# Optimization experiments

Measured on AMD Instinct MI355X. Metric: run time of the kernel, lower is better.

Reference implementation:

```python
import jax, jax.numpy as jnp
import numpy as np
from jax import lax

RADIUS = 5


def setup_inputs() -> dict:
    key = jax.random.key(0)
    k1, k2 = jax.random.split(key)
    B, K, H, W = 4, 6, 128, 128
    win = 2 * RADIUS + 1
    labels = jax.random.uniform(k1, (B, K, H, W), dtype=jnp.float32)
    weights = jax.random.uniform(k2, (B, H * W, win, win), dtype=jnp.float32)
    return {"labels": labels, "weights": weights}


def reference(labels, weights):
    # labels:  [B, K, H, W]  class probabilities
    B, K, H, W = labels.shape
    win = 2 * RADIUS + 1
    N = H * W

    # Extract 11x11 patches around every pixel for all classes at once.
    patches = lax.conv_general_dilated_patches(
        labels, (win, win), (1, 1), padding=[(RADIUS, RADIUS), (RADIUS, RADIUS)]
    )
    patches = patches.reshape(B, K, win * win, N)

    w = weights.reshape(B, N, win * win)

    # sum over window of weights * P, per class: wp[b,k,n] = sum_o w[b,n,o] * patches[b,k,o,n]
    wp = jnp.einsum('bkon,bno->bkn', patches, w)

    p = labels.reshape(B, K, N)
    num = jnp.einsum('bkn,bkn->bk', p, wp)          # association
    den = jnp.einsum('bkn,bn->bk', p, w.sum(-1))    # degree
    L = num / den                                    # [B, K]

    # nn.L1Loss()(L, zeros) per class = mean_b |L[b,k]|
    losses = jnp.mean(jnp.abs(L), axis=0)            # [K]
    return K - jnp.sum(losses)
```

## Files before the change

kernel.cpp:

```cpp
#include <hip/hip_runtime.h>

#define RADIUS 5
#define WIN    11
#define WIN2   121
#define KCLS   6
#define HH     128
#define WW     128
#define BB     4
#define NPIX   (HH*WW)
#define TPB    256
#define NBLK   (BB*HH)
#define LABW   138
#define NSITE  (WIN*LABW)
#define PLSTR  (NSITE*2)

__global__ __launch_bounds__(TPB, 2) void ncut_main(
    const float* __restrict__ labels,
    const float* __restrict__ weights,
    float* __restrict__ part) {
  __shared__ float shl[3 * PLSTR];
  __shared__ float shred[4 * 12];

  const int tid = threadIdx.x;
  const int blk = blockIdx.x;
  const int b   = blk >> 7;
  const int y0  = blk & (HH - 1);

  const float* labB = labels + (size_t)b * KCLS * NPIX;
  for (int s = tid; s < NSITE; s += TPB) {
    const int tr = s / LABW;
    const int tc = s - tr * LABW;
    const int gy = y0 - RADIUS + tr;
    const int gx = tc - RADIUS;
    const bool ok = ((unsigned)gy < (unsigned)HH) & ((unsigned)gx < (unsigned)WW);
    const float* lp = labB + (size_t)gy * WW + gx;
#pragma unroll
    for (int p = 0; p < 3; ++p) {
      float2 v = make_float2(0.f, 0.f);
      if (ok) {
        v.x = lp[(size_t)(2 * p) * NPIX];
        v.y = lp[(size_t)(2 * p + 1) * NPIX];
      }
      *reinterpret_cast<float2*>(shl + p * PLSTR + 2 * s) = v;
    }
  }
  __syncthreads();

  const int px = tid >> 1;
  const int q  = tid & 1;
  const float* wr = weights +
      ((size_t)b * NPIX + (size_t)y0 * WW + px) * WIN2 + q * 60;

  float2 a0 = make_float2(0.f, 0.f);
  float2 a1 = make_float2(0.f, 0.f);
  float2 a2 = make_float2(0.f, 0.f);
  float wsum = 0.f;

#pragma unroll
  for (int g = 0; g < 15; ++g) {
    float4 wv;
    __builtin_memcpy(&wv, wr + 4 * g, 16);
#pragma unroll
    for (int m = 0; m < 4; ++m) {
      const int c  = 4 * g + m;
      const int liA = (c / WIN) * LABW + (c % WIN);
      const int liB = ((60 + c) / WIN) * LABW + ((60 + c) % WIN);
      const int li  = px + (q ? liB : liA);
      const float w = (m == 0) ? wv.x : (m == 1) ? wv.y : (m == 2) ? wv.z : wv.w;
      wsum += w;
      const float2 v0 = *reinterpret_cast<const float2*>(shl + 0 * PLSTR + 2 * li);
      const float2 v1 = *reinterpret_cast<const float2*>(shl + 1 * PLSTR + 2 * li);
      const float2 v2 = *reinterpret_cast<const float2*>(shl + 2 * PLSTR + 2 * li);
      a0.x += w * v0.x; a0.y += w * v0.y;
      a1.x += w * v1.x; a1.y += w * v1.y;
      a2.x += w * v2.x; a2.y += w * v2.y;
    }
  }
  if (q == 0) {
    const float w = wr[120];
    const int li = px + 10 * LABW + 10;
    wsum += w;
    const float2 v0 = *reinterpret_cast<const float2*>(shl + 0 * PLSTR + 2 * li);
    const float2 v1 = *reinterpret_cast<const float2*>(shl + 1 * PLSTR + 2 * li);
    const float2 v2 = *reinterpret_cast<const float2*>(shl + 2 * PLSTR + 2 * li);
    a0.x += w * v0.x; a0.y += w * v0.y;
    a1.x += w * v1.x; a1.y += w * v1.y;
    a2.x += w * v2.x; a2.y += w * v2.y;
  }

  wsum += __shfl_xor(wsum, 1);
  a0.x += __shfl_xor(a0.x, 1); a0.y += __shfl_xor(a0.y, 1);
  a1.x += __shfl_xor(a1.x, 1); a1.y += __shfl_xor(a1.y, 1);
  a2.x += __shfl_xor(a2.x, 1); a2.y += __shfl_xor(a2.y, 1);

  const int lc = px + 5 * LABW + 5;
  const float2 c0 = *reinterpret_cast<const float2*>(shl + 0 * PLSTR + 2 * lc);
  const float2 c1 = *reinterpret_cast<const float2*>(shl + 1 * PLSTR + 2 * lc);
  const float2 c2 = *reinterpret_cast<const float2*>(shl + 2 * PLSTR + 2 * lc);
  float nv[KCLS] = {c0.x * a0.x, c0.y * a0.y, c1.x * a1.x,
                    c1.y * a1.y, c2.x * a2.x, c2.y * a2.y};
  float dv[KCLS] = {c0.x * wsum, c0.y * wsum, c1.x * wsum,
                    c1.y * wsum, c2.x * wsum, c2.y * wsum};

#pragma unroll
  for (int off = 2; off <= 32; off <<= 1) {
#pragma unroll
    for (int k = 0; k < KCLS; ++k) {
      nv[k] += __shfl_xor(nv[k], off);
      dv[k] += __shfl_xor(dv[k], off);
    }
  }
  const int wave = tid >> 6;
  if ((tid & 63) == 0) {
#pragma unroll
    for (int k = 0; k < KCLS; ++k) {
      shred[wave * 12 + k]     = nv[k];
      shred[wave * 12 + 6 + k] = dv[k];
    }
  }
  __syncthreads();
  if (tid < 12) {
    float s = 0.f;
#pragma unroll
    for (int w = 0; w < 4; ++w) s += shred[w * 12 + tid];
    part[blk * 12 + tid] = s;
  }
}

__global__ __launch_bounds__(256) void ncut_final(
    const float* __restrict__ part, float* __restrict__ out) {
  __shared__ float shf[8 * 48];
  const int t   = threadIdx.x;
  const int seg = t >> 5;
  const int bk  = t & 31;
  if (bk < 24) {
    const int b = bk / KCLS;
    const int k = bk - b * KCLS;
    const int r0 = b * HH + seg * 16;
    float num = 0.f, den = 0.f;
#pragma unroll 4
    for (int i = 0; i < 16; ++i) {
      const float* p = part + (size_t)(r0 + i) * 12;
      num += p[k];
      den += p[6 + k];
    }
    shf[seg * 48 + bk * 2]     = num;
    shf[seg * 48 + bk * 2 + 1] = den;
  }
  __syncthreads();
  float val = 0.f;
  if (t < 24) {
    float n = 0.f, d = 0.f;
#pragma unroll
    for (int s = 0; s < 8; ++s) {
      n += shf[s * 48 + t * 2];
      d += shf[s * 48 + t * 2 + 1];
    }
    val = fabsf(n / d) * (1.0f / BB);
  }
  if (t < 64) {
#pragma unroll
    for (int off = 16; off; off >>= 1) val += __shfl_down(val, off);
    if (t == 0) out[0] = (float)KCLS - val;
  }
}

extern "C" void kernel_launch(void* const* d_in, const int* in_sizes, int n_in,
                              void* d_out, int out_size, void* d_ws, size_t ws_size,
                              hipStream_t stream) {
  const float* labels  = (const float*)d_in[0];
  const float* weights = (const float*)d_in[1];
  float* out  = (float*)d_out;
  float* part = (float*)d_ws;

  ncut_main<<<NBLK, TPB, 0, stream>>>(labels, weights, part);
  ncut_final<<<1, 256, 0, stream>>>(part, out);
}
```

Measured before the change: 22.29 us.

## Split rows into half-width blocks with four threads per pixel interleaved

Each block now covers 64 pixels of a row instead of 128, which doubles the block count and shrinks the shared-memory halo tile. Four threads share each pixel and take window taps interleaved (stride 4), so adjacent lanes read consecutive weight floats for better coalescing. The shuffle reductions and the final kernel are updated for the new layout. In exchange, the halo overhead per block grows, loads drop from float4 to scalar, and the final reduction reads twice as many partials.

```diff
diff --git a/kernel.cpp b/kernel.cpp
--- a/kernel.cpp
+++ b/kernel.cpp
@@ -9,12 +9,13 @@
 #define BB     4
 #define NPIX   (HH*WW)
 #define TPB    256
-#define NBLK   (BB*HH)
-#define LABW   138
+#define NBLK   (BB*HH*2)
+#define PXB    64
+#define LABW   (PXB + 2*RADIUS)
 #define NSITE  (WIN*LABW)
 #define PLSTR  (NSITE*2)
 
-__global__ __launch_bounds__(TPB, 2) void ncut_main(
+__global__ __launch_bounds__(TPB, 4) void ncut_main(
     const float* __restrict__ labels,
     const float* __restrict__ weights,
     float* __restrict__ part) {
@@ -23,15 +24,17 @@
 
   const int tid = threadIdx.x;
   const int blk = blockIdx.x;
-  const int b   = blk >> 7;
-  const int y0  = blk & (HH - 1);
+  const int b   = blk >> 8;
+  const int rem = blk & 255;
+  const int y0  = rem >> 1;
+  const int x0  = (rem & 1) * PXB;
 
   const float* labB = labels + (size_t)b * KCLS * NPIX;
   for (int s = tid; s < NSITE; s += TPB) {
     const int tr = s / LABW;
     const int tc = s - tr * LABW;
     const int gy = y0 - RADIUS + tr;
-    const int gx = tc - RADIUS;
+    const int gx = x0 + tc - RADIUS;
     const bool ok = ((unsigned)gy < (unsigned)HH) & ((unsigned)gx < (unsigned)WW);
     const float* lp = labB + (size_t)gy * WW + gx;
 #pragma unroll
@@ -46,10 +49,10 @@
   }
   __syncthreads();
 
-  const int px = tid >> 1;
-  const int q  = tid & 1;
-  const float* wr = weights +
-      ((size_t)b * NPIX + (size_t)y0 * WW + px) * WIN2 + q * 60;
+  const int px = tid >> 2;
+  const int q  = tid & 3;
+  const float* wrowq = weights +
+      ((size_t)b * NPIX + (size_t)y0 * WW + x0 + px) * WIN2 + q;
 
   float2 a0 = make_float2(0.f, 0.f);
   float2 a1 = make_float2(0.f, 0.f);
@@ -57,27 +60,23 @@
   float wsum = 0.f;
 
 #pragma unroll
-  for (int g = 0; g < 15; ++g) {
-    float4 wv;
-    __builtin_memcpy(&wv, wr + 4 * g, 16);
-#pragma unroll
-    for (int m = 0; m < 4; ++m) {
-      const int c  = 4 * g + m;
-      const int liA = (c / WIN) * LABW + (c % WIN);
-      const int liB = ((60 + c) / WIN) * LABW + ((60 + c) % WIN);
-      const int li  = px + (q ? liB : liA);
-      const float w = (m == 0) ? wv.x : (m == 1) ? wv.y : (m == 2) ? wv.z : wv.w;
-      wsum += w;
-      const float2 v0 = *reinterpret_cast<const float2*>(shl + 0 * PLSTR + 2 * li);
-      const float2 v1 = *reinterpret_cast<const float2*>(shl + 1 * PLSTR + 2 * li);
-      const float2 v2 = *reinterpret_cast<const float2*>(shl + 2 * PLSTR + 2 * li);
-      a0.x += w * v0.x; a0.y += w * v0.y;
-      a1.x += w * v1.x; a1.y += w * v1.y;
-      a2.x += w * v2.x; a2.y += w * v2.y;
-    }
+  for (int j = 0; j < 30; ++j) {
+    const int o4 = 4 * j;
+    const int S  = (o4 / WIN) * LABW + (o4 % WIN);
+    const int Wn = WIN - (o4 % WIN);
+    const float w = wrowq[o4];
+    wsum += w;
+    int li = px + S + q;
+    if (Wn < 4) li += (q >= Wn) ? (LABW - WIN) : 0;
+    const float2 v0 = *reinterpret_cast<const float2*>(shl + 0 * PLSTR + 2 * li);
+    const float2 v1 = *reinterpret_cast<const float2*>(shl + 1 * PLSTR + 2 * li);
+    const float2 v2 = *reinterpret_cast<const float2*>(shl + 2 * PLSTR + 2 * li);
+    a0.x += w * v0.x; a0.y += w * v0.y;
+    a1.x += w * v1.x; a1.y += w * v1.y;
+    a2.x += w * v2.x; a2.y += w * v2.y;
   }
   if (q == 0) {
-    const float w = wr[120];
+    const float w = wrowq[120];
     const int li = px + 10 * LABW + 10;
     wsum += w;
     const float2 v0 = *reinterpret_cast<const float2*>(shl + 0 * PLSTR + 2 * li);
@@ -88,10 +87,13 @@
     a2.x += w * v2.x; a2.y += w * v2.y;
   }
 
-  wsum += __shfl_xor(wsum, 1);
-  a0.x += __shfl_xor(a0.x, 1); a0.y += __shfl_xor(a0.y, 1);
-  a1.x += __shfl_xor(a1.x, 1); a1.y += __shfl_xor(a1.y, 1);
-  a2.x += __shfl_xor(a2.x, 1); a2.y += __shfl_xor(a2.y, 1);
+#pragma unroll
+  for (int off = 1; off <= 2; off <<= 1) {
+    wsum += __shfl_xor(wsum, off);
+    a0.x += __shfl_xor(a0.x, off); a0.y += __shfl_xor(a0.y, off);
+    a1.x += __shfl_xor(a1.x, off); a1.y += __shfl_xor(a1.y, off);
+    a2.x += __shfl_xor(a2.x, off); a2.y += __shfl_xor(a2.y, off);
+  }
 
   const int lc = px + 5 * LABW + 5;
   const float2 c0 = *reinterpret_cast<const float2*>(shl + 0 * PLSTR + 2 * lc);
@@ -103,7 +105,7 @@
                     c1.y * wsum, c2.x * wsum, c2.y * wsum};
 
 #pragma unroll
-  for (int off = 2; off <= 32; off <<= 1) {
+  for (int off = 4; off <= 32; off <<= 1) {
 #pragma unroll
     for (int k = 0; k < KCLS; ++k) {
       nv[k] += __shfl_xor(nv[k], off);
@@ -136,10 +138,10 @@
   if (bk < 24) {
     const int b = bk / KCLS;
     const int k = bk - b * KCLS;
-    const int r0 = b * HH + seg * 16;
+    const int r0 = b * 256 + seg * 32;
     float num = 0.f, den = 0.f;
 #pragma unroll 4
-    for (int i = 0; i < 16; ++i) {
+    for (int i = 0; i < 32; ++i) {
       const float* p = part + (size_t)(r0 + i) * 12;
       num += p[k];
       den += p[6 + k];
```

Measured after the change: 20.18 us. 1.1x faster.
